# Optimization experiments

Hardware: AMD Instinct MI355X
Metric: run time of the kernel (lower is better)

## Reference

```python
import jax, jax.numpy as jnp
import numpy as np

TOKEN_DIM = 256
NUM_HEADS = 2
IN_DIMS = 512
D = TOKEN_DIM * NUM_HEADS  # 512
SCALE = TOKEN_DIM ** (-0.5)


def _l2norm(v, axis):
    # torch F.normalize: v / max(||v||_2, eps)
    n = jnp.sqrt(jnp.sum(v * v, axis=axis, keepdims=True))
    return v / jnp.maximum(n, 1e-12)


def setup_inputs() -> dict:
    key = jax.random.key(0)
    ks = jax.random.split(key, 10)
    b, n = 8, 4096
    x = jax.random.normal(ks[0], (b, n, IN_DIMS), dtype=jnp.float32)
    s = 0.02
    Wq = jax.random.normal(ks[1], (IN_DIMS, D), dtype=jnp.float32) * s
    bq = jax.random.normal(ks[2], (D,), dtype=jnp.float32) * s
    Wk = jax.random.normal(ks[3], (IN_DIMS, D), dtype=jnp.float32) * s
    bk = jax.random.normal(ks[4], (D,), dtype=jnp.float32) * s
    Wr = jax.random.normal(ks[5], (D, TOKEN_DIM), dtype=jnp.float32) * s
    br = jax.random.normal(ks[6], (TOKEN_DIM,), dtype=jnp.float32) * s
    w_alpha = jax.random.normal(ks[7], (D, 1), dtype=jnp.float32)
    w_beta = jax.random.normal(ks[8], (D, 1), dtype=jnp.float32)
    return {"x": x, "Wq": Wq, "bq": bq, "Wk": Wk, "bk": bk,
            "Wr": Wr, "br": br, "w_alpha": w_alpha, "w_beta": w_beta}


def reference(x, Wq, bq, Wk, bk, Wr, br, w_alpha, w_beta):
    # x: [b, n, in_dims]
    q = x @ Wq + bq                      # [b, n, D]
    k = x @ Wk + bk                      # [b, n, D]
    q = _l2norm(q, axis=-1)
    k = _l2norm(k, axis=-1)
    v = _l2norm(k, axis=-1)              # original bug: value = normalize(key)

    alpha_w = (q @ w_alpha) * SCALE      # [b, n, 1]
    alpha_w = _l2norm(alpha_w, axis=1)   # normalize over token axis
    g_q = jnp.sum(alpha_w * q, axis=1)   # [b, D]
    g_q = jax.nn.softmax(g_q, axis=-1)

    p = g_q[:, None, :] * k              # [b, n, D]
    beta_w = _l2norm((p @ w_beta) * SCALE, axis=1)  # [b, n, 1]
    g_k = jnp.sum(beta_w * p, axis=1)    # [b, D]
    g_k = jax.nn.softmax(g_k, axis=-1)

    kvi = g_k[:, None, :] * v + q        # [b, n, D]
    return kvi @ Wr + br                 # [b, n, token_dim]
```

## Files before the change

### kernel.cpp

```cpp
#include <hip/hip_runtime.h>
#include <hip/hip_bf16.h>
#include <stdint.h>

#define BATCH    8
#define NTOKB    4096
#define NTOK     (BATCH * NTOKB)
#define DIN      512
#define DD       512
#define TD       256
#define SCALE    0.0625f
#define LSTR     36

typedef unsigned short ushortT;
typedef __attribute__((ext_vector_type(8))) short  short8;
typedef __attribute__((ext_vector_type(4))) float  f32x4;

union Frag { uint4 u; short8 s; };

__device__ __forceinline__ float bf_lo(uint32_t u) { return __uint_as_float(u << 16); }
__device__ __forceinline__ float bf_hi(uint32_t u) { return __uint_as_float(u & 0xffff0000u); }
__device__ __forceinline__ float bf2f(ushortT u) { return __uint_as_float(((uint32_t)u) << 16); }
__device__ __forceinline__ ushortT f2bf(float f) {
    uint32_t u = __float_as_uint(f);
    return (ushortT)((u + 0x7fffu + ((u >> 16) & 1u)) >> 16);
}
__device__ __forceinline__ short8 lds_frag(const ushortT* p) {
    uint2 a = *reinterpret_cast<const uint2*>(p);
    uint2 b = *reinterpret_cast<const uint2*>(p + 4);
    Frag f; f.u.x = a.x; f.u.y = a.y; f.u.z = b.x; f.u.w = b.y;
    return f.s;
}
__device__ __forceinline__ void gload_lds16(const ushortT* g, ushortT* l) {
    __builtin_amdgcn_global_load_lds(
        (const __attribute__((address_space(1))) uint32_t*)(const void*)g,
        (__attribute__((address_space(3))) uint32_t*)(void*)l,
        16, 0, 0);
}

__global__ __launch_bounds__(256) void packw_kernel(
    const float* __restrict__ Wq, const float* __restrict__ Wk,
    const float* __restrict__ Wr, ushortT* __restrict__ W16)
{
    const int blk = blockIdx.x;
    if (blk < 32) {
        const int mat = blk >> 4, c = blk & 15;
        const float* S = mat ? Wk : Wq;
        ushortT* D = W16 + (size_t)mat * (512 * 512) + (size_t)c * 16384;
        for (int i = threadIdx.x; i < 16384; i += 256) {
            int n = i & 511, p = i >> 9;
            int l = ((p >> 3) ^ ((n >> 1) & 3)) * 8 + (p & 7);
            D[n * 32 + p] = f2bf(S[(size_t)(c * 32 + l) * 512 + n]);
        }
    } else {
        const int c = blk - 32;
        ushortT* D = W16 + (size_t)2 * (512 * 512) + (size_t)c * 8192;
        for (int i = threadIdx.x; i < 8192; i += 256) {
            int n = i & 255, p = i >> 8;
            int l = ((p >> 3) ^ ((n >> 1) & 3)) * 8 + (p & 7);
            D[n * 32 + p] = f2bf(Wr[(size_t)(c * 32 + l) * 256 + n]);
        }
    }
}

__global__ __launch_bounds__(512) void gemm_qk_kernel(
    const float* __restrict__ x, const ushortT* __restrict__ W16,
    const float* __restrict__ bq, const float* __restrict__ bk,
    const float* __restrict__ w_alpha,
    ushortT* __restrict__ qn, ushortT* __restrict__ kn,
    float* __restrict__ alpha_raw)
{
    __shared__ __align__(16) ushortT xs[64 * LSTR];
    __shared__ __align__(16) ushortT wsd[512 * 32];
    __shared__ float rowsq[8][64];
    __shared__ float alphap[8][64];
    __shared__ float rnorm_s[64];

    const int tid = threadIdx.x;
    const int mat = blockIdx.y;
    const size_t tok0 = (size_t)blockIdx.x * 64;
    const ushortT* Wb = W16 + (size_t)mat * (512 * 512);
    const float* bias = mat ? bk : bq;
    ushortT* dst = mat ? kn : qn;

    const int lane = tid & 63, w = tid >> 6;
    const int m = lane & 15, quad = lane >> 4;

    f32x4 acc[4][4];
    #pragma unroll
    for (int tr = 0; tr < 4; ++tr)
        #pragma unroll
        for (int tc = 0; tc < 4; ++tc) acc[tr][tc] = (f32x4){0.f, 0.f, 0.f, 0.f};

    const int xtok = tid >> 3;
    const int xkg  = (tid & 7) * 4;
    const float* xsrc = x + (tok0 + xtok) * DIN;

    for (int c = 0; c < 16; ++c) {
        __syncthreads();
        {
            float4 xv = *reinterpret_cast<const float4*>(xsrc + c * 32 + xkg);
            ushort4 xb;
            xb.x = f2bf(xv.x); xb.y = f2bf(xv.y); xb.z = f2bf(xv.z); xb.w = f2bf(xv.w);
            *reinterpret_cast<ushort4*>(&xs[xtok * LSTR + xkg]) = xb;
        }
        {
            const ushortT* wsrc = Wb + (size_t)c * 16384;
            #pragma unroll
            for (int i = 0; i < 4; ++i) {
                const int region = i * 8 + w;
                gload_lds16(wsrc + region * 512 + lane * 8, &wsd[region * 512]);
            }
        }
        __syncthreads();
        {
            short8 af[4], bf[4];
            #pragma unroll
            for (int tr = 0; tr < 4; ++tr)
                af[tr] = lds_frag(&xs[(tr * 16 + m) * LSTR + quad * 8]);
            #pragma unroll
            for (int tc = 0; tc < 4; ++tc) {
                const int n = w * 64 + tc * 16 + m;
                bf[tc] = *reinterpret_cast<const short8*>(
                    &wsd[n * 32 + ((quad ^ ((n >> 1) & 3)) * 8)]);
            }
            #pragma unroll
            for (int tr = 0; tr < 4; ++tr)
                #pragma unroll
                for (int tc = 0; tc < 4; ++tc)
                    acc[tr][tc] = __builtin_amdgcn_mfma_f32_16x16x32_bf16(af[tr], bf[tc], acc[tr][tc], 0, 0, 0);
        }
    }

    float biasv[4], wa[4];
    #pragma unroll
    for (int tc = 0; tc < 4; ++tc) {
        biasv[tc] = bias[w * 64 + tc * 16 + m];
        wa[tc] = (mat == 0) ? w_alpha[w * 64 + tc * 16 + m] : 0.f;
    }
    #pragma unroll
    for (int tr = 0; tr < 4; ++tr)
        #pragma unroll
        for (int tc = 0; tc < 4; ++tc)
            #pragma unroll
            for (int reg = 0; reg < 4; ++reg)
                acc[tr][tc][reg] += biasv[tc];

    __syncthreads();
    #pragma unroll
    for (int tr = 0; tr < 4; ++tr) {
        #pragma unroll
        for (int reg = 0; reg < 4; ++reg) {
            float s = 0.f, a = 0.f;
            #pragma unroll
            for (int tc = 0; tc < 4; ++tc) {
                float v = acc[tr][tc][reg];
                s = fmaf(v, v, s);
                a = fmaf(v, wa[tc], a);
            }
            #pragma unroll
            for (int off = 1; off < 16; off <<= 1) {
                s += __shfl_xor(s, off);
                a += __shfl_xor(a, off);
            }
            if (m == 0) {
                rowsq[w][tr * 16 + quad * 4 + reg] = s;
                alphap[w][tr * 16 + quad * 4 + reg] = a;
            }
        }
    }
    __syncthreads();
    if (tid < 64) {
        float ss = 0.f, aa = 0.f;
        #pragma unroll
        for (int w2 = 0; w2 < 8; ++w2) { ss += rowsq[w2][tid]; aa += alphap[w2][tid]; }
        float rn = 1.0f / fmaxf(sqrtf(ss), 1e-12f);
        rnorm_s[tid] = rn;
        if (mat == 0) alpha_raw[tok0 + tid] = SCALE * aa * rn;
    }
    __syncthreads();
    #pragma unroll
    for (int tr = 0; tr < 4; ++tr) {
        #pragma unroll
        for (int reg = 0; reg < 4; ++reg) {
            float rn = rnorm_s[tr * 16 + quad * 4 + reg];
            size_t row = tok0 + tr * 16 + quad * 4 + reg;
            ushortT* rp = dst + row * DD + w * 64 + m;
            #pragma unroll
            for (int tc = 0; tc < 4; ++tc)
                rp[tc * 16] = f2bf(acc[tr][tc][reg] * rn);
        }
    }
}

__global__ __launch_bounds__(256) void norm_kernel(const float* __restrict__ in,
                                                   float* __restrict__ inv_out)
{
    int b = blockIdx.x;
    __shared__ float red[256];
    float s = 0.f;
    for (int i = threadIdx.x; i < NTOKB; i += 256) {
        float v = in[b * NTOKB + i];
        s = fmaf(v, v, s);
    }
    red[threadIdx.x] = s;
    __syncthreads();
    for (int off = 128; off > 0; off >>= 1) {
        if (threadIdx.x < off) red[threadIdx.x] += red[threadIdx.x + off];
        __syncthreads();
    }
    if (threadIdx.x == 0) inv_out[b] = 1.0f / fmaxf(sqrtf(red[0]), 1e-12f);
}

__global__ __launch_bounds__(256) void wsum_kernel(const ushortT* __restrict__ M,
                                                   const float* __restrict__ raw,
                                                   const float* __restrict__ invp,
                                                   float* __restrict__ dst)
{
    const int blk = blockIdx.x, tid = threadIdx.x;
    const int b = blk >> 5;
    const int i0 = (blk & 31) * 128;
    __shared__ float wr[128];
    if (tid < 128) wr[tid] = raw[(size_t)b * NTOKB + i0 + tid];
    __syncthreads();
    const uint32_t* M32 = reinterpret_cast<const uint32_t*>(M);
    size_t base = ((size_t)b * NTOKB + i0) * 256 + tid;
    float a0 = 0.f, a1 = 0.f;
    for (int ii = 0; ii < 128; ++ii) {
        uint32_t v = M32[base + (size_t)ii * 256];
        float wv = wr[ii];
        a0 = fmaf(wv, bf_lo(v), a0);
        a1 = fmaf(wv, bf_hi(v), a1);
    }
    float iv = invp[b];
    atomicAdd(&dst[b * DD + 2 * tid],     a0 * iv);
    atomicAdd(&dst[b * DD + 2 * tid + 1], a1 * iv);
}

__global__ __launch_bounds__(256) void softmax_kernel(const float* __restrict__ in,
                                                      const float* __restrict__ mul,
                                                      const float* __restrict__ wbeta,
                                                      float* __restrict__ out,
                                                      float* __restrict__ wb2)
{
    int b = blockIdx.x, tid = threadIdx.x;
    __shared__ float red[256];
    float v0 = in[b * DD + tid], v1 = in[b * DD + 256 + tid];
    if (mul) { v0 *= mul[b * DD + tid]; v1 *= mul[b * DD + 256 + tid]; }
    red[tid] = fmaxf(v0, v1);
    __syncthreads();
    for (int off = 128; off > 0; off >>= 1) {
        if (tid < off) red[tid] = fmaxf(red[tid], red[tid + off]);
        __syncthreads();
    }
    float m = red[0];
    __syncthreads();
    float e0 = expf(v0 - m), e1 = expf(v1 - m);
    red[tid] = e0 + e1;
    __syncthreads();
    for (int off = 128; off > 0; off >>= 1) {
        if (tid < off) red[tid] += red[tid + off];
        __syncthreads();
    }
    float rs = 1.0f / red[0];
    float o0 = e0 * rs, o1 = e1 * rs;
    out[b * DD + tid] = o0;
    out[b * DD + 256 + tid] = o1;
    if (wb2) {
        wb2[b * DD + tid]       = o0 * wbeta[tid];
        wb2[b * DD + 256 + tid] = o1 * wbeta[256 + tid];
    }
}

__global__ __launch_bounds__(256) void beta_kernel(const ushortT* __restrict__ kn,
                                                   const float* __restrict__ wb2,
                                                   float* __restrict__ beta_raw)
{
    int wave = threadIdx.x >> 6, lane = threadIdx.x & 63;
    size_t tok = (size_t)blockIdx.x * 4 + wave;
    int b = (int)(tok >> 12);
    uint4 kv = *reinterpret_cast<const uint4*>(kn + tok * DD + lane * 8);
    float4 wv0 = *reinterpret_cast<const float4*>(wb2 + b * DD + lane * 8);
    float4 wv1 = *reinterpret_cast<const float4*>(wb2 + b * DD + lane * 8 + 4);
    float s = bf_lo(kv.x) * wv0.x + bf_hi(kv.x) * wv0.y
            + bf_lo(kv.y) * wv0.z + bf_hi(kv.y) * wv0.w
            + bf_lo(kv.z) * wv1.x + bf_hi(kv.z) * wv1.y
            + bf_lo(kv.w) * wv1.z + bf_hi(kv.w) * wv1.w;
    #pragma unroll
    for (int off = 32; off > 0; off >>= 1) s += __shfl_xor(s, off);
    if (lane == 0) beta_raw[tok] = SCALE * s;
}

__global__ __launch_bounds__(256) void out_mfma_kernel(
    const ushortT* __restrict__ qn, const ushortT* __restrict__ kn,
    const float* __restrict__ g_k, const ushortT* __restrict__ WrT,
    const float* __restrict__ br, float* __restrict__ out)
{
    __shared__ __align__(16) ushortT kvs[64 * LSTR];
    __shared__ __align__(16) ushortT wrs[256 * 32];
    __shared__ float gks[512];

    const int tid = threadIdx.x;
    const size_t tok0 = (size_t)blockIdx.x * 64;
    const int b = (int)(tok0 >> 12);

    gks[tid] = g_k[b * DD + tid];
    gks[256 + tid] = g_k[b * DD + 256 + tid];

    const int lane = tid & 63, w = tid >> 6;
    const int m = lane & 15, quad = lane >> 4;

    f32x4 acc[4][4];
    #pragma unroll
    for (int tr = 0; tr < 4; ++tr)
        #pragma unroll
        for (int tc = 0; tc < 4; ++tc) acc[tr][tc] = (f32x4){0.f, 0.f, 0.f, 0.f};

    const int st  = tid >> 2;
    const int skg = (tid & 3) * 8;

    for (int c = 0; c < 16; ++c) {
        __syncthreads();
        {
            const size_t base = (tok0 + st) * DD + c * 32 + skg;
            uint4 qv = *reinterpret_cast<const uint4*>(qn + base);
            uint4 kv = *reinterpret_cast<const uint4*>(kn + base);
            const float* g = &gks[c * 32 + skg];
            ushortT o[8];
            o[0] = f2bf(fmaf(g[0], bf_lo(kv.x), bf_lo(qv.x)));
            o[1] = f2bf(fmaf(g[1], bf_hi(kv.x), bf_hi(qv.x)));
            o[2] = f2bf(fmaf(g[2], bf_lo(kv.y), bf_lo(qv.y)));
            o[3] = f2bf(fmaf(g[3], bf_hi(kv.y), bf_hi(qv.y)));
            o[4] = f2bf(fmaf(g[4], bf_lo(kv.z), bf_lo(qv.z)));
            o[5] = f2bf(fmaf(g[5], bf_hi(kv.z), bf_hi(qv.z)));
            o[6] = f2bf(fmaf(g[6], bf_lo(kv.w), bf_lo(qv.w)));
            o[7] = f2bf(fmaf(g[7], bf_hi(kv.w), bf_hi(qv.w)));
            uint2* lp = reinterpret_cast<uint2*>(&kvs[st * LSTR + skg]);
            lp[0] = make_uint2(((uint32_t)o[1] << 16) | o[0], ((uint32_t)o[3] << 16) | o[2]);
            lp[1] = make_uint2(((uint32_t)o[5] << 16) | o[4], ((uint32_t)o[7] << 16) | o[6]);
        }
        {
            const ushortT* wsrc = WrT + (size_t)c * 8192;
            #pragma unroll
            for (int i = 0; i < 4; ++i) {
                const int region = i * 4 + w;
                gload_lds16(wsrc + region * 512 + lane * 8, &wrs[region * 512]);
            }
        }
        __syncthreads();
        {
            short8 af[4], bfr[4];
            #pragma unroll
            for (int tr = 0; tr < 4; ++tr)
                af[tr] = lds_frag(&kvs[(tr * 16 + m) * LSTR + quad * 8]);
            #pragma unroll
            for (int tc = 0; tc < 4; ++tc) {
                const int n = w * 64 + tc * 16 + m;
                bfr[tc] = *reinterpret_cast<const short8*>(
                    &wrs[n * 32 + ((quad ^ ((n >> 1) & 3)) * 8)]);
            }
            #pragma unroll
            for (int tr = 0; tr < 4; ++tr)
                #pragma unroll
                for (int tc = 0; tc < 4; ++tc)
                    acc[tr][tc] = __builtin_amdgcn_mfma_f32_16x16x32_bf16(af[tr], bfr[tc], acc[tr][tc], 0, 0, 0);
        }
    }

    float brv[4];
    #pragma unroll
    for (int tc = 0; tc < 4; ++tc) brv[tc] = br[w * 64 + tc * 16 + m];
    #pragma unroll
    for (int tr = 0; tr < 4; ++tr) {
        #pragma unroll
        for (int reg = 0; reg < 4; ++reg) {
            size_t row = tok0 + tr * 16 + quad * 4 + reg;
            float* rp = out + row * TD + w * 64 + m;
            #pragma unroll
            for (int tc = 0; tc < 4; ++tc)
                rp[tc * 16] = acc[tr][tc][reg] + brv[tc];
        }
    }
}

extern "C" void kernel_launch(void* const* d_in, const int* in_sizes, int n_in,
                              void* d_out, int out_size, void* d_ws, size_t ws_size,
                              hipStream_t stream)
{
    const float* x       = (const float*)d_in[0];
    const float* Wq      = (const float*)d_in[1];
    const float* bq      = (const float*)d_in[2];
    const float* Wk      = (const float*)d_in[3];
    const float* bk      = (const float*)d_in[4];
    const float* Wr      = (const float*)d_in[5];
    const float* br      = (const float*)d_in[6];
    const float* w_alpha = (const float*)d_in[7];
    const float* w_beta  = (const float*)d_in[8];
    float* out = (float*)d_out;

    ushortT* kn = (ushortT*)d_out;

    char* ws = (char*)d_ws;
    ushortT* qn = (ushortT*)ws;        ws += (size_t)NTOK * DD * sizeof(ushortT);
    ushortT* W16 = (ushortT*)ws;       ws += (size_t)2 * 512 * 512 * sizeof(ushortT)
                                           + (size_t)512 * 256 * sizeof(ushortT);
    float* alpha_raw = (float*)ws;     ws += (size_t)NTOK * sizeof(float);
    float* beta_raw  = (float*)ws;     ws += (size_t)NTOK * sizeof(float);
    float* gq_raw = (float*)ws;        ws += (size_t)BATCH * DD * sizeof(float);
    float* h_raw  = (float*)ws;        ws += (size_t)BATCH * DD * sizeof(float);
    float* g_q    = (float*)ws;        ws += (size_t)BATCH * DD * sizeof(float);
    float* wb2    = (float*)ws;        ws += (size_t)BATCH * DD * sizeof(float);
    float* g_k    = (float*)ws;        ws += (size_t)BATCH * DD * sizeof(float);
    float* inv_a  = (float*)ws;        ws += 64;
    float* inv_b  = (float*)ws;        ws += 64;
    ushortT* WrT = W16 + (size_t)2 * 512 * 512;

    hipMemsetAsync(gq_raw, 0, 2 * BATCH * DD * sizeof(float), stream);

    packw_kernel<<<48, 256, 0, stream>>>(Wq, Wk, Wr, W16);
    gemm_qk_kernel<<<dim3(NTOK / 64, 2), 512, 0, stream>>>(x, W16, bq, bk, w_alpha, qn, kn, alpha_raw);
    norm_kernel<<<BATCH, 256, 0, stream>>>(alpha_raw, inv_a);
    wsum_kernel<<<256, 256, 0, stream>>>(qn, alpha_raw, inv_a, gq_raw);
    softmax_kernel<<<BATCH, 256, 0, stream>>>(gq_raw, nullptr, w_beta, g_q, wb2);
    beta_kernel<<<NTOK / 4, 256, 0, stream>>>(kn, wb2, beta_raw);
    norm_kernel<<<BATCH, 256, 0, stream>>>(beta_raw, inv_b);
    wsum_kernel<<<256, 256, 0, stream>>>(kn, beta_raw, inv_b, h_raw);
    softmax_kernel<<<BATCH, 256, 0, stream>>>(h_raw, g_q, nullptr, g_k, nullptr);
    out_mfma_kernel<<<NTOK / 64, 256, 0, stream>>>(qn, kn, g_k, WrT, br, out);
}
```

Measured before the change: 247.7 us.

## Double-buffer LDS tiles in QK and output GEMM kernels to overlap loads with MFMA

Both MFMA GEMM kernels now use two LDS buffers for the activation and weight tiles. The next K-chunk's global loads (direct-to-LDS weight loads plus register-held activation loads) are issued before the current chunk's MFMAs, and the converted activations are written to the alternate buffer afterwards. This halves the barriers per iteration and hides global latency behind compute. In exchange LDS use roughly doubles (about 36 KB more per block in the QK kernel), which may reduce occupancy.

```diff
diff --git a/kernel.cpp b/kernel.cpp
--- a/kernel.cpp
+++ b/kernel.cpp
@@ -69,8 +69,8 @@
     ushortT* __restrict__ qn, ushortT* __restrict__ kn,
     float* __restrict__ alpha_raw)
 {
-    __shared__ __align__(16) ushortT xs[64 * LSTR];
-    __shared__ __align__(16) ushortT wsd[512 * 32];
+    __shared__ __align__(16) ushortT xs[2][64 * LSTR];
+    __shared__ __align__(16) ushortT wsd[2][512 * 32];
     __shared__ float rowsq[8][64];
     __shared__ float alphap[8][64];
     __shared__ float rnorm_s[64];
@@ -95,40 +95,55 @@
     const int xkg  = (tid & 7) * 4;
     const float* xsrc = x + (tok0 + xtok) * DIN;
 
+    {
+        float4 xv = *reinterpret_cast<const float4*>(xsrc + 0 * 32 + xkg);
+        const ushortT* wsrc = Wb;
+        #pragma unroll
+        for (int i = 0; i < 4; ++i) {
+            const int region = i * 8 + w;
+            gload_lds16(wsrc + region * 512 + lane * 8, &wsd[0][region * 512]);
+        }
+        ushort4 xb;
+        xb.x = f2bf(xv.x); xb.y = f2bf(xv.y); xb.z = f2bf(xv.z); xb.w = f2bf(xv.w);
+        *reinterpret_cast<ushort4*>(&xs[0][xtok * LSTR + xkg]) = xb;
+    }
+    __syncthreads();
+
     for (int c = 0; c < 16; ++c) {
-        __syncthreads();
-        {
-            float4 xv = *reinterpret_cast<const float4*>(xsrc + c * 32 + xkg);
-            ushort4 xb;
-            xb.x = f2bf(xv.x); xb.y = f2bf(xv.y); xb.z = f2bf(xv.z); xb.w = f2bf(xv.w);
-            *reinterpret_cast<ushort4*>(&xs[xtok * LSTR + xkg]) = xb;
-        }
-        {
-            const ushortT* wsrc = Wb + (size_t)c * 16384;
+        const int cur = c & 1, nxt = cur ^ 1;
+        float4 xv;
+        if (c + 1 < 16) {
+            xv = *reinterpret_cast<const float4*>(xsrc + (c + 1) * 32 + xkg);
+            const ushortT* wsrc = Wb + (size_t)(c + 1) * 16384;
             #pragma unroll
             for (int i = 0; i < 4; ++i) {
                 const int region = i * 8 + w;
-                gload_lds16(wsrc + region * 512 + lane * 8, &wsd[region * 512]);
-            }
-        }
-        __syncthreads();
+                gload_lds16(wsrc + region * 512 + lane * 8, &wsd[nxt][region * 512]);
+            }
+        }
         {
-            short8 af[4], bf[4];
+            short8 af[4], bfv[4];
             #pragma unroll
             for (int tr = 0; tr < 4; ++tr)
-                af[tr] = lds_frag(&xs[(tr * 16 + m) * LSTR + quad * 8]);
+                af[tr] = lds_frag(&xs[cur][(tr * 16 + m) * LSTR + quad * 8]);
             #pragma unroll
             for (int tc = 0; tc < 4; ++tc) {
                 const int n = w * 64 + tc * 16 + m;
-                bf[tc] = *reinterpret_cast<const short8*>(
-                    &wsd[n * 32 + ((quad ^ ((n >> 1) & 3)) * 8)]);
+                bfv[tc] = *reinterpret_cast<const short8*>(
+                    &wsd[cur][n * 32 + ((quad ^ ((n >> 1) & 3)) * 8)]);
             }
             #pragma unroll
             for (int tr = 0; tr < 4; ++tr)
                 #pragma unroll
                 for (int tc = 0; tc < 4; ++tc)
-                    acc[tr][tc] = __builtin_amdgcn_mfma_f32_16x16x32_bf16(af[tr], bf[tc], acc[tr][tc], 0, 0, 0);
-        }
+                    acc[tr][tc] = __builtin_amdgcn_mfma_f32_16x16x32_bf16(af[tr], bfv[tc], acc[tr][tc], 0, 0, 0);
+        }
+        if (c + 1 < 16) {
+            ushort4 xb;
+            xb.x = f2bf(xv.x); xb.y = f2bf(xv.y); xb.z = f2bf(xv.z); xb.w = f2bf(xv.w);
+            *reinterpret_cast<ushort4*>(&xs[nxt][xtok * LSTR + xkg]) = xb;
+        }
+        __syncthreads();
     }
 
     float biasv[4], wa[4];
@@ -145,7 +160,6 @@
             for (int reg = 0; reg < 4; ++reg)
                 acc[tr][tc][reg] += biasv[tc];
 
-    __syncthreads();
     #pragma unroll
     for (int tr = 0; tr < 4; ++tr) {
         #pragma unroll
@@ -295,8 +309,8 @@
     const float* __restrict__ g_k, const ushortT* __restrict__ WrT,
     const float* __restrict__ br, float* __restrict__ out)
 {
-    __shared__ __align__(16) ushortT kvs[64 * LSTR];
-    __shared__ __align__(16) ushortT wrs[256 * 32];
+    __shared__ __align__(16) ushortT kvs[2][64 * LSTR];
+    __shared__ __align__(16) ushortT wrs[2][256 * 32];
     __shared__ float gks[512];
 
     const int tid = threadIdx.x;
@@ -317,14 +331,67 @@
 
     const int st  = tid >> 2;
     const int skg = (tid & 3) * 8;
+    const size_t tbase = (tok0 + st) * DD + skg;
+
+    uint4 qv = *reinterpret_cast<const uint4*>(qn + tbase);
+    uint4 kv = *reinterpret_cast<const uint4*>(kn + tbase);
+    {
+        const ushortT* wsrc = WrT;
+        #pragma unroll
+        for (int i = 0; i < 4; ++i) {
+            const int region = i * 4 + w;
+            gload_lds16(wsrc + region * 512 + lane * 8, &wrs[0][region * 512]);
+        }
+    }
+    __syncthreads();
+    {
+        const float* g = &gks[skg];
+        ushortT o[8];
+        o[0] = f2bf(fmaf(g[0], bf_lo(kv.x), bf_lo(qv.x)));
+        o[1] = f2bf(fmaf(g[1], bf_hi(kv.x), bf_hi(qv.x)));
+        o[2] = f2bf(fmaf(g[2], bf_lo(kv.y), bf_lo(qv.y)));
+        o[3] = f2bf(fmaf(g[3], bf_hi(kv.y), bf_hi(qv.y)));
+        o[4] = f2bf(fmaf(g[4], bf_lo(kv.z), bf_lo(qv.z)));
+        o[5] = f2bf(fmaf(g[5], bf_hi(kv.z), bf_hi(qv.z)));
+        o[6] = f2bf(fmaf(g[6], bf_lo(kv.w), bf_lo(qv.w)));
+        o[7] = f2bf(fmaf(g[7], bf_hi(kv.w), bf_hi(qv.w)));
+        uint2* lp = reinterpret_cast<uint2*>(&kvs[0][st * LSTR + skg]);
+        lp[0] = make_uint2(((uint32_t)o[1] << 16) | o[0], ((uint32_t)o[3] << 16) | o[2]);
+        lp[1] = make_uint2(((uint32_t)o[5] << 16) | o[4], ((uint32_t)o[7] << 16) | o[6]);
+    }
+    __syncthreads();
 
     for (int c = 0; c < 16; ++c) {
-        __syncthreads();
+        const int cur = c & 1, nxt = cur ^ 1;
+        if (c + 1 < 16) {
+            qv = *reinterpret_cast<const uint4*>(qn + tbase + (c + 1) * 32);
+            kv = *reinterpret_cast<const uint4*>(kn + tbase + (c + 1) * 32);
+            const ushortT* wsrc = WrT + (size_t)(c + 1) * 8192;
+            #pragma unroll
+            for (int i = 0; i < 4; ++i) {
+                const int region = i * 4 + w;
+                gload_lds16(wsrc + region * 512 + lane * 8, &wrs[nxt][region * 512]);
+            }
+        }
         {
-            const size_t base = (tok0 + st) * DD + c * 32 + skg;
-            uint4 qv = *reinterpret_cast<const uint4*>(qn + base);
-            uint4 kv = *reinterpret_cast<const uint4*>(kn + base);
-            const float* g = &gks[c * 32 + skg];
+            short8 af[4], bfr[4];
+            #pragma unroll
+            for (int tr = 0; tr < 4; ++tr)
+                af[tr] = lds_frag(&kvs[cur][(tr * 16 + m) * LSTR + quad * 8]);
+            #pragma unroll
+            for (int tc = 0; tc < 4; ++tc) {
+                const int n = w * 64 + tc * 16 + m;
+                bfr[tc] = *reinterpret_cast<const short8*>(
+                    &wrs[cur][n * 32 + ((quad ^ ((n >> 1) & 3)) * 8)]);
+            }
+            #pragma unroll
+            for (int tr = 0; tr < 4; ++tr)
+                #pragma unroll
+                for (int tc = 0; tc < 4; ++tc)
+                    acc[tr][tc] = __builtin_amdgcn_mfma_f32_16x16x32_bf16(af[tr], bfr[tc], acc[tr][tc], 0, 0, 0);
+        }
+        if (c + 1 < 16) {
+            const float* g = &gks[(c + 1) * 32 + skg];
             ushortT o[8];
             o[0] = f2bf(fmaf(g[0], bf_lo(kv.x), bf_lo(qv.x)));
             o[1] = f2bf(fmaf(g[1], bf_hi(kv.x), bf_hi(qv.x)));
@@ -334,36 +401,11 @@
             o[5] = f2bf(fmaf(g[5], bf_hi(kv.z), bf_hi(qv.z)));
             o[6] = f2bf(fmaf(g[6], bf_lo(kv.w), bf_lo(qv.w)));
             o[7] = f2bf(fmaf(g[7], bf_hi(kv.w), bf_hi(qv.w)));
-            uint2* lp = reinterpret_cast<uint2*>(&kvs[st * LSTR + skg]);
+            uint2* lp = reinterpret_cast<uint2*>(&kvs[nxt][st * LSTR + skg]);
             lp[0] = make_uint2(((uint32_t)o[1] << 16) | o[0], ((uint32_t)o[3] << 16) | o[2]);
             lp[1] = make_uint2(((uint32_t)o[5] << 16) | o[4], ((uint32_t)o[7] << 16) | o[6]);
         }
-        {
-            const ushortT* wsrc = WrT + (size_t)c * 8192;
-            #pragma unroll
-            for (int i = 0; i < 4; ++i) {
-                const int region = i * 4 + w;
-                gload_lds16(wsrc + region * 512 + lane * 8, &wrs[region * 512]);
-            }
-        }
         __syncthreads();
-        {
-            short8 af[4], bfr[4];
-            #pragma unroll
-            for (int tr = 0; tr < 4; ++tr)
-                af[tr] = lds_frag(&kvs[(tr * 16 + m) * LSTR + quad * 8]);
-            #pragma unroll
-            for (int tc = 0; tc < 4; ++tc) {
-                const int n = w * 64 + tc * 16 + m;
-                bfr[tc] = *reinterpret_cast<const short8*>(
-                    &wrs[n * 32 + ((quad ^ ((n >> 1) & 3)) * 8)]);
-            }
-            #pragma unroll
-            for (int tr = 0; tr < 4; ++tr)
-                #pragma unroll
-                for (int tc = 0; tc < 4; ++tc)
-                    acc[tr][tc] = __builtin_amdgcn_mfma_f32_16x16x32_bf16(af[tr], bfr[tc], acc[tr][tc], 0, 0, 0);
-        }
     }
 
     float brv[4];
```

Measured after the change: 254.1 us. 1.03x slower.
